# Optimization experiments

Measured on AMD Instinct MI355X. Metric: run time of the kernel, lower is better.

The kernel has to match this reference:

```python
import jax, jax.numpy as jnp
import numpy as np

# Dimensions (match init_kwargs / input_specs)
B, C, H, W = 16, 96, 224, 224
COUT = 96
PH, PW = 16, 16          # patch_size (== patch_stride, non-overlapping)
KH, KW = 3, 3            # patch_kernel and output_kernel
PAD = 1                  # padding
GH, GW = H // PH, W // PW
P = GH * GW              # num_patches = 196


def setup_inputs() -> dict:
    key = jax.random.key(0)
    k1, k2, k3 = jax.random.split(key, 3)
    x = jax.random.normal(k1, (B, C, H, W), dtype=jnp.float32)
    # kaiming-normal-ish init scales (fan_in over trailing dims, as torch does)
    pf = jax.random.normal(k2, (C, P, 1, KH, KW), dtype=jnp.float32) * np.float32(np.sqrt(2.0 / (P * KH * KW)))
    of = jax.random.normal(k3, (COUT, C, KH, KW), dtype=jnp.float32) * np.float32(np.sqrt(2.0 / (C * KH * KW)))
    return {"x": x, "patch_filters": pf, "output_filters": of}


def _self_conv2d(x, patch_filters):
    """Locally-connected per-patch depthwise conv.

    x: (B, C, H, W); patch_filters: (C, P, 1, KH, KW).
    Each of the P non-overlapping PHxPW patches of each channel is convolved
    with its own KHxKW kernel (padding=PAD, stride=1), then patches are
    reassembled into the full (B, C, H, W) map.
    """
    # (B, C, GH, PH, GW, PW) -> (B, C, GH, GW, PH, PW) -> (B, C*P, PH, PW)
    xp = x.reshape(B, C, GH, PH, GW, PW).transpose(0, 1, 2, 4, 3, 5).reshape(B, C * P, PH, PW)
    k = patch_filters.reshape(C * P, 1, KH, KW)
    y = jax.lax.conv_general_dilated(
        xp, k,
        window_strides=(1, 1),
        padding=[(PAD, PAD), (PAD, PAD)],
        feature_group_count=C * P,
        dimension_numbers=("NCHW", "OIHW", "NCHW"),
    )  # (B, C*P, PH, PW) since 3x3 conv with pad 1 preserves size
    return y.reshape(B, C, GH, GW, PH, PW).transpose(0, 1, 2, 4, 3, 5).reshape(B, C, H, W)


def reference(x, patch_filters, output_filters):
    # input already at (max_input_height, max_input_width) -> F.pad is a no-op
    sa = _self_conv2d(x, patch_filters)
    out = jax.lax.conv_general_dilated(
        sa, output_filters,
        window_strides=(1, 1),
        padding=[(PAD, PAD), (PAD, PAD)],
        dimension_numbers=("NCHW", "OIHW", "NCHW"),
    )  # (B, COUT, H, W)
    return jax.nn.gelu(out, approximate=False)  # torch nn.GELU() = exact erf gelu
```

## Files before the change

### kernel.cpp

```cpp
#include <hip/hip_runtime.h>
#include <hip/hip_bf16.h>

#define B_    16
#define C_    96
#define H_    224
#define W_    224
#define COUT_ 96
#define GH_   14
#define GW_   14
#define P_    196
#define HW_   (H_*W_)
#define NCH_  12

#define AS1 __attribute__((address_space(1)))
#define AS3 __attribute__((address_space(3)))

typedef __attribute__((ext_vector_type(8))) unsigned short ushort8;
typedef __attribute__((ext_vector_type(8))) short        short8;
typedef __attribute__((ext_vector_type(4))) float        f32x4;

__device__ __forceinline__ unsigned short f2bf(float f) {
    union { __hip_bfloat16 h; unsigned short u; } cv;
    cv.h = __float2bfloat16(f);
    return cv.u;
}

__global__ __launch_bounds__(256) void prep_ofb(const float* __restrict__ of,
                                                unsigned short* __restrict__ ofb3,
                                                unsigned short* __restrict__ zp) {
    if (blockIdx.x == 0 && threadIdx.x < 128) zp[threadIdx.x] = 0;
    int e = blockIdx.x * 256 + threadIdx.x;
    if (e < 82944) {
        int j    = e & 7;
        int l    = (e >> 3) & 63;
        int ni   = (e >> 9) % 6;
        int cs   = (e / 3072) % 3;
        int tap  = e / 9216;
        int cout = ni * 16 + (l & 15);
        int c    = cs * 32 + (l >> 4) * 8 + j;
        ofb3[e] = f2bf(of[((size_t)cout * 96 + c) * 9 + tap]);
    }
}

__global__ __launch_bounds__(256) void sa_kernel(const float* __restrict__ x,
                                                 const float* __restrict__ pf,
                                                 unsigned short* __restrict__ sa) {
    int bid   = blockIdx.x;
    int patch = bid % P_;
    int b     = bid / P_;
    int gh = patch / GW_, gw = patch % GW_;
    int t  = threadIdx.x;
    int py = t >> 4, px = t & 15;
    int y  = gh * 16 + py, xx = gw * 16 + px;

    __shared__ float xs[2][8][256];

    const float* xp0 = x + (size_t)b * C_ * HW_ + (size_t)y * W_ + xx;

    float lf[8];
    #pragma unroll
    for (int ch = 0; ch < 8; ++ch) lf[ch] = xp0[(size_t)ch * HW_];

    for (int cc = 0; cc < NCH_; ++cc) {
        int buf = cc & 1;
        #pragma unroll
        for (int ch = 0; ch < 8; ++ch) xs[buf][ch][t] = lf[ch];
        __syncthreads();
        if (cc < NCH_ - 1) {
            #pragma unroll
            for (int ch = 0; ch < 8; ++ch)
                lf[ch] = xp0[(size_t)((cc + 1) * 8 + ch) * HW_];
        }

        ushort8 v;
        #pragma unroll
        for (int ch = 0; ch < 8; ++ch) {
            const float* wgt = pf + ((size_t)(cc * 8 + ch) * P_ + patch) * 9;
            float a = 0.f;
            #pragma unroll
            for (int dy = -1; dy <= 1; ++dy) {
                int yy = py + dy;
                if ((unsigned)yy < 16u) {
                    #pragma unroll
                    for (int dx = -1; dx <= 1; ++dx) {
                        int xq = px + dx;
                        if ((unsigned)xq < 16u)
                            a = fmaf(xs[buf][ch][yy * 16 + xq],
                                     wgt[(dy + 1) * 3 + (dx + 1)], a);
                    }
                }
            }
            v[ch] = f2bf(a);
        }
        *(ushort8*)&sa[(((size_t)(b * NCH_ + cc) * H_ + y) * W_ + xx) * 8] = v;
    }
}

__global__ __launch_bounds__(256, 2) void conv2_mfma(const unsigned short* __restrict__ sa,
                                                     const unsigned short* __restrict__ ofb3,
                                                     const unsigned short* __restrict__ zp,
                                                     float* __restrict__ out) {
    int bid0 = blockIdx.x;
    int bid  = (bid0 % 8) * (3136 / 8) + bid0 / 8;
    int patch = bid % P_;
    int b     = bid / P_;
    int gh = patch / GW_, gw = patch % GW_;
    int y0 = gh * 16, x0 = gw * 16;

    int t = threadIdx.x;
    int w = t >> 6, l = t & 63;
    int mrow = l & 15, kgrp = l >> 4;

    __shared__ ushort8 at8[4352];

    #pragma unroll
    for (int i = 0; i < 17; ++i) {
        int v = t + i * 256;
        const unsigned short* src = zp;
        if (v < 4212) {
            int hpx = v / 13, ccl = v - hpx * 13;
            if (ccl < 12) {
                int gy = y0 - 1 + hpx / 18, gx = x0 - 1 + hpx % 18;
                if ((unsigned)gy < (unsigned)H_ && (unsigned)gx < (unsigned)W_)
                    src = &sa[(((size_t)(b * NCH_ + ccl) * H_ + gy) * W_ + gx) * 8];
            }
        }
        __builtin_amdgcn_global_load_lds((const AS1 unsigned int*)src,
                                         (AS3 unsigned int*)&at8[v], 16, 0, 0);
    }

    f32x4 acc[4][6];
    #pragma unroll
    for (int mi = 0; mi < 4; ++mi)
        #pragma unroll
        for (int ni = 0; ni < 6; ++ni)
            acc[mi][ni] = (f32x4)0.f;

    __syncthreads();

    const unsigned short* at = (const unsigned short*)at8;

    short8 bfA[6], bfB[6];
    auto LOADBF = [&](short8* dst, int T) {
        const unsigned short* p = ofb3 + (size_t)(T / 3) * 9216 + (T % 3) * 3072 + l * 8;
        #pragma unroll
        for (int ni = 0; ni < 6; ++ni)
            dst[ni] = *(const short8*)&p[ni * 512];
    };

    LOADBF(bfA, 0);
    #pragma unroll
    for (int T = 0; T < 27; ++T) {
        short8* cur = (T & 1) ? bfB : bfA;
        short8* nxt = (T & 1) ? bfA : bfB;
        if (T + 1 < 27) LOADBF(nxt, T + 1);
        __builtin_amdgcn_sched_barrier(0);

        int tap = T / 3, cs = T % 3;
        int ky = tap / 3, kx = tap % 3;
        #pragma unroll
        for (int mi = 0; mi < 4; ++mi) {
            short8 af = *(const short8*)&at[((w * 4 + mi + ky) * 18 + kx + mrow) * 104
                                            + (cs * 4 + kgrp) * 8];
            #pragma unroll
            for (int ni = 0; ni < 6; ++ni)
                acc[mi][ni] = __builtin_amdgcn_mfma_f32_16x16x32_bf16(
                    af, cur[ni], acc[mi][ni], 0, 0, 0);
        }
    }

    #pragma unroll
    for (int mi = 0; mi < 4; ++mi) {
        int gy = y0 + w * 4 + mi;
        #pragma unroll
        for (int ni = 0; ni < 6; ++ni) {
            int cout = ni * 16 + mrow;
            f32x4 gv;
            #pragma unroll
            for (int j = 0; j < 4; ++j) {
                float vv = acc[mi][ni][j];
                gv[j] = 0.5f * vv * (1.0f + erff(vv * 0.70710678118f));
            }
            *(f32x4*)&out[((size_t)b * COUT_ + cout) * HW_ + (size_t)gy * W_ +
                          x0 + kgrp * 4] = gv;
        }
    }
}

extern "C" void kernel_launch(void* const* d_in, const int* in_sizes, int n_in,
                              void* d_out, int out_size, void* d_ws, size_t ws_size,
                              hipStream_t stream) {
    const float* x  = (const float*)d_in[0];
    const float* pf = (const float*)d_in[1];
    const float* of = (const float*)d_in[2];
    float* out = (float*)d_out;

    unsigned short* sa   = (unsigned short*)d_ws;
    unsigned short* ofb3 = (unsigned short*)((char*)d_ws + 154140672);
    unsigned short* zp   = (unsigned short*)((char*)d_ws + 154306560);

    prep_ofb<<<324, 256, 0, stream>>>(of, ofb3, zp);
    sa_kernel<<<B_ * P_, 256, 0, stream>>>(x, pf, sa);
    conv2_mfma<<<B_ * P_, 256, 0, stream>>>(sa, ofb3, zp, out);
}
```

Before: 355.8 us.

## Split conv2 tiles into half-patches and split output channels across waves

The output conv kernel now processes half of a 16x16 patch (8 rows) per block, doubling the grid. The four waves are arranged 2x2 over rows and output channels instead of each wave covering all 96 channels. That halves accumulator registers and LDS per block so the launch bound can allow 3 blocks per SM. The LDS layout changes to channel-chunk-major with no padding slot. The cost is more halo reloading (10 of 18 rows per half) and each wave reusing B fragments over fewer rows.

```diff
diff --git a/kernel.cpp b/kernel.cpp
--- a/kernel.cpp
+++ b/kernel.cpp
@@ -96,56 +96,58 @@
     }
 }
 
-__global__ __launch_bounds__(256, 2) void conv2_mfma(const unsigned short* __restrict__ sa,
+__global__ __launch_bounds__(256, 3) void conv2_mfma(const unsigned short* __restrict__ sa,
                                                      const unsigned short* __restrict__ ofb3,
                                                      const unsigned short* __restrict__ zp,
                                                      float* __restrict__ out) {
     int bid0 = blockIdx.x;
-    int bid  = (bid0 % 8) * (3136 / 8) + bid0 / 8;
-    int patch = bid % P_;
-    int b     = bid / P_;
+    int bid  = (bid0 % 8) * (6272 / 8) + bid0 / 8;
+    int half = bid & 1;
+    int pid  = bid >> 1;
+    int patch = pid % P_;
+    int b     = pid / P_;
     int gh = patch / GW_, gw = patch % GW_;
-    int y0 = gh * 16, x0 = gw * 16;
+    int y0 = gh * 16 + half * 8, x0 = gw * 16;
 
     int t = threadIdx.x;
     int w = t >> 6, l = t & 63;
+    int wm = w & 1, wn = w >> 1;
     int mrow = l & 15, kgrp = l >> 4;
 
-    __shared__ ushort8 at8[4352];
-
-    #pragma unroll
-    for (int i = 0; i < 17; ++i) {
+    __shared__ ushort8 at8[2304];
+
+    #pragma unroll
+    for (int i = 0; i < 9; ++i) {
         int v = t + i * 256;
         const unsigned short* src = zp;
-        if (v < 4212) {
-            int hpx = v / 13, ccl = v - hpx * 13;
-            if (ccl < 12) {
-                int gy = y0 - 1 + hpx / 18, gx = x0 - 1 + hpx % 18;
-                if ((unsigned)gy < (unsigned)H_ && (unsigned)gx < (unsigned)W_)
-                    src = &sa[(((size_t)(b * NCH_ + ccl) * H_ + gy) * W_ + gx) * 8];
-            }
+        if (v < 2160) {
+            int ccl = v / 180, hpx = v - ccl * 180;
+            int gy = y0 - 1 + hpx / 18, gx = x0 - 1 + hpx % 18;
+            if ((unsigned)gy < (unsigned)H_ && (unsigned)gx < (unsigned)W_)
+                src = &sa[(((size_t)(b * NCH_ + ccl) * H_ + gy) * W_ + gx) * 8];
         }
         __builtin_amdgcn_global_load_lds((const AS1 unsigned int*)src,
                                          (AS3 unsigned int*)&at8[v], 16, 0, 0);
     }
 
-    f32x4 acc[4][6];
+    f32x4 acc[4][3];
     #pragma unroll
     for (int mi = 0; mi < 4; ++mi)
         #pragma unroll
-        for (int ni = 0; ni < 6; ++ni)
+        for (int ni = 0; ni < 3; ++ni)
             acc[mi][ni] = (f32x4)0.f;
 
     __syncthreads();
 
     const unsigned short* at = (const unsigned short*)at8;
 
-    short8 bfA[6], bfB[6];
+    short8 bfA[3], bfB[3];
     auto LOADBF = [&](short8* dst, int T) {
-        const unsigned short* p = ofb3 + (size_t)(T / 3) * 9216 + (T % 3) * 3072 + l * 8;
-        #pragma unroll
-        for (int ni = 0; ni < 6; ++ni)
-            dst[ni] = *(const short8*)&p[ni * 512];
+        const unsigned short* p = ofb3 + (size_t)(T / 3) * 9216 + (T % 3) * 3072
+                                  + (wn * 3) * 512 + l * 8;
+        #pragma unroll
+        for (int nj = 0; nj < 3; ++nj)
+            dst[nj] = *(const short8*)&p[nj * 512];
     };
 
     LOADBF(bfA, 0);
@@ -160,25 +162,26 @@
         int ky = tap / 3, kx = tap % 3;
         #pragma unroll
         for (int mi = 0; mi < 4; ++mi) {
-            short8 af = *(const short8*)&at[((w * 4 + mi + ky) * 18 + kx + mrow) * 104
-                                            + (cs * 4 + kgrp) * 8];
-            #pragma unroll
-            for (int ni = 0; ni < 6; ++ni)
-                acc[mi][ni] = __builtin_amdgcn_mfma_f32_16x16x32_bf16(
-                    af, cur[ni], acc[mi][ni], 0, 0, 0);
+            short8 af = *(const short8*)&at[((cs * 4 + kgrp) * 180
+                                            + (wm * 4 + mi + ky) * 18
+                                            + kx + mrow) * 8];
+            #pragma unroll
+            for (int nj = 0; nj < 3; ++nj)
+                acc[mi][nj] = __builtin_amdgcn_mfma_f32_16x16x32_bf16(
+                    af, cur[nj], acc[mi][nj], 0, 0, 0);
         }
     }
 
     #pragma unroll
     for (int mi = 0; mi < 4; ++mi) {
-        int gy = y0 + w * 4 + mi;
-        #pragma unroll
-        for (int ni = 0; ni < 6; ++ni) {
-            int cout = ni * 16 + mrow;
+        int gy = y0 + wm * 4 + mi;
+        #pragma unroll
+        for (int nj = 0; nj < 3; ++nj) {
+            int cout = (wn * 3 + nj) * 16 + mrow;
             f32x4 gv;
             #pragma unroll
             for (int j = 0; j < 4; ++j) {
-                float vv = acc[mi][ni][j];
+                float vv = acc[mi][nj][j];
                 gv[j] = 0.5f * vv * (1.0f + erff(vv * 0.70710678118f));
             }
             *(f32x4*)&out[((size_t)b * COUT_ + cout) * HW_ + (size_t)gy * W_ +
@@ -201,5 +204,5 @@
 
     prep_ofb<<<324, 256, 0, stream>>>(of, ofb3, zp);
     sa_kernel<<<B_ * P_, 256, 0, stream>>>(x, pf, sa);
-    conv2_mfma<<<B_ * P_, 256, 0, stream>>>(sa, ofb3, zp, out);
-}
+    conv2_mfma<<<B_ * P_ * 2, 256, 0, stream>>>(sa, ofb3, zp, out);
+}
```

New measurement: 382.2 us. 7.4% more time.
